# Performance work log

Hardware: AMD Instinct MI355X
Metric: run time of the kernel (lower is better)

## Reference

```python
import jax, jax.numpy as jnp
import numpy as np

V, E, H, S, B, T = 32000, 256, 512, 128, 32, 32


def setup_inputs() -> dict:
    key = jax.random.key(0)
    ks = iter(jax.random.split(key, 32))

    def w(shape, s=0.05):
        return jax.random.normal(next(ks), shape, dtype=jnp.float32) * s

    return dict(
        src=jax.random.randint(next(ks), (S, B), 0, V),
        trg=jax.random.randint(next(ks), (T, B), 0, V),
        embed=w((V, E)),
        enc_Wih_f=w((4 * H, E)), enc_Whh_f=w((4 * H, H)), enc_bih_f=w((4 * H,)), enc_bhh_f=w((4 * H,)),
        enc_Wih_b=w((4 * H, E)), enc_Whh_b=w((4 * H, H)), enc_bih_b=w((4 * H,)), enc_bhh_b=w((4 * H,)),
        attn_W=w((H, 2 * H)), attn_b=w((H,)), attn_v=w((H,)),
        dec_Wih0=w((4 * H, H + E)), dec_Whh0=w((4 * H, H)), dec_bih0=w((4 * H,)), dec_bhh0=w((4 * H,)),
        dec_Wih1=w((4 * H, H)), dec_Whh1=w((4 * H, H)), dec_bih1=w((4 * H,)), dec_bhh1=w((4 * H,)),
        out_W=w((V, 2 * H)), out_b=w((V,)),
    )


def _cell(x, h, c, Wih, Whh, bih, bhh):
    # PyTorch LSTM gate order: i, f, g, o
    z = x @ Wih.T + h @ Whh.T + bih + bhh
    i, f, g, o = jnp.split(z, 4, axis=-1)
    c2 = jax.nn.sigmoid(f) * c + jax.nn.sigmoid(i) * jnp.tanh(g)
    h2 = jax.nn.sigmoid(o) * jnp.tanh(c2)
    return h2, c2


def _run_lstm(xs, Wih, Whh, bih, bhh):
    # xs: [S, B, in]; returns outputs [S,B,H], final (h,c)
    h0 = jnp.zeros((xs.shape[1], Whh.shape[1]), xs.dtype)

    def step(carry, x):
        h, c = carry
        h2, c2 = _cell(x, h, c, Wih, Whh, bih, bhh)
        return (h2, c2), h2

    (hT, cT), outs = jax.lax.scan(step, (h0, h0), xs)
    return outs, hT, cT


def _forward(src, trg, embed,
             enc_Wih_f, enc_Whh_f, enc_bih_f, enc_bhh_f,
             enc_Wih_b, enc_Whh_b, enc_bih_b, enc_bhh_b,
             attn_W, attn_b, attn_v,
             dec_Wih0, dec_Whh0, dec_bih0, dec_bhh0,
             dec_Wih1, dec_Whh1, dec_bih1, dec_bhh1,
             out_W, out_b):
    emb_src = embed[src]                                  # [S,B,E]
    # bidirectional 1-layer encoder LSTM
    f_outs, hf, cf = _run_lstm(emb_src, enc_Wih_f, enc_Whh_f, enc_bih_f, enc_bhh_f)
    b_outs, hb, cb = _run_lstm(emb_src[::-1], enc_Wih_b, enc_Whh_b, enc_bih_b, enc_bhh_b)
    enc_out = f_outs + b_outs[::-1]                       # [S,B,H] (sum of directions)
    h = jnp.stack([hf, hb])                               # [2,B,H] -> decoder init state
    c = jnp.stack([cf, cb])
    enc_bsh = enc_out.transpose(1, 0, 2)                  # [B,S,H]

    def dec_step(carry, tok):
        h, c = carry
        emb = embed[tok]                                  # [B,E]
        q = h[-1]                                         # top-layer hidden [B,H]
        qs = jnp.broadcast_to(q[:, None, :], enc_bsh.shape)
        energy = jnp.tanh(jnp.concatenate([qs, enc_bsh], -1) @ attn_W.T + attn_b)  # [B,S,H]
        scores = energy @ attn_v                          # [B,S]
        aw = jax.nn.softmax(scores, axis=1)
        ctx = jnp.einsum('bs,bsh->bh', aw, enc_bsh)       # [B,H]
        x = jnp.concatenate([emb, ctx], -1)               # [B,E+H]
        h0, c0 = _cell(x, h[0], c[0], dec_Wih0, dec_Whh0, dec_bih0, dec_bhh0)
        h1, c1 = _cell(h0, h[1], c[1], dec_Wih1, dec_Whh1, dec_bih1, dec_bhh1)
        logits = jax.nn.log_softmax(
            jnp.concatenate([h1, ctx], -1) @ out_W.T + out_b, axis=-1)             # [B,V]
        return (jnp.stack([h0, h1]), jnp.stack([c0, c1])), logits

    # teacher forcing (ratio=1.0): input at step t is trg[t-1]
    _, outs = jax.lax.scan(dec_step, (h, c), trg[:-1])    # [T-1,B,V]
    outputs = jnp.concatenate(
        [jnp.zeros((1,) + outs.shape[1:], outs.dtype), outs], 0)  # outputs[0]=0 as in torch
    return outputs


def reference(src, trg, embed,
              enc_Wih_f, enc_Whh_f, enc_bih_f, enc_bhh_f,
              enc_Wih_b, enc_Whh_b, enc_bih_b, enc_bhh_b,
              attn_W, attn_b, attn_v,
              dec_Wih0, dec_Whh0, dec_bih0, dec_bhh0,
              dec_Wih1, dec_Whh1, dec_bih1, dec_bhh1,
              out_W, out_b):
    return _forward(src, trg, embed,
                    enc_Wih_f, enc_Whh_f, enc_bih_f, enc_bhh_f,
                    enc_Wih_b, enc_Whh_b, enc_bih_b, enc_bhh_b,
                    attn_W, attn_b, attn_v,
                    dec_Wih0, dec_Whh0, dec_bih0, dec_bhh0,
                    dec_Wih1, dec_Whh1, dec_bih1, dec_bhh1,
                    out_W, out_b)
```

## Files before the change

### kernel.cpp

```cpp
#include <hip/hip_runtime.h>
#include <stdint.h>


using short8 = __attribute__((ext_vector_type(8))) short;
using f32x4  = __attribute__((ext_vector_type(4))) float;
typedef _Float16 half2v __attribute__((ext_vector_type(2)));

__device__ __forceinline__ short f2bf(float x){
  unsigned u = __float_as_uint(x);
  unsigned r = (u + 0x7fffu + ((u >> 16) & 1u)) >> 16;
  return (short)(unsigned short)r;
}
__device__ __forceinline__ float bf2f_lo(unsigned u){ return __uint_as_float(u << 16); }
__device__ __forceinline__ float bf2f_hi(unsigned u){ return __uint_as_float(u & 0xffff0000u); }
__device__ __forceinline__ float sigmf(float x){ return 1.0f/(1.0f + __expf(-x)); }
__device__ __forceinline__ float fast_tanh(float x){
  const float e = __expf(2.0f*x);
  return 1.0f - 2.0f/(e + 1.0f);
}
__device__ __forceinline__ unsigned pack_h2(float a, float b){
  unsigned short ha = __builtin_bit_cast(unsigned short, (_Float16)a);
  unsigned short hb = __builtin_bit_cast(unsigned short, (_Float16)b);
  return (unsigned)ha | ((unsigned)hb << 16);
}
__device__ __forceinline__ float h2lo(unsigned u){ return (float)__builtin_bit_cast(half2v,u)[0]; }
__device__ __forceinline__ float h2hi(unsigned u){ return (float)__builtin_bit_cast(half2v,u)[1]; }
__device__ __forceinline__ float dot2u(unsigned x, unsigned w, float c){
#if __has_builtin(__builtin_amdgcn_fdot2)
  return __builtin_amdgcn_fdot2(__builtin_bit_cast(half2v,x), __builtin_bit_cast(half2v,w), c, false);
#else
  half2v hx = __builtin_bit_cast(half2v,x), hw = __builtin_bit_cast(half2v,w);
  c = fmaf((float)hx[0], (float)hw[0], c);
  c = fmaf((float)hx[1], (float)hw[1], c);
  return c;
#endif
}

__device__ __forceinline__ float4 load_coh_f4(const float* p){
  float4 v;
  asm volatile("global_load_dwordx4 %0, %1, off sc0 sc1\n\ts_waitcnt vmcnt(0)"
               : "=&v"(v) : "v"(p) : "memory");
  return v;
}
__device__ __forceinline__ uint4 load_coh_u4(const unsigned* p){
  uint4 v;
  asm volatile("global_load_dwordx4 %0, %1, off sc0 sc1\n\ts_waitcnt vmcnt(0)"
               : "=&v"(v) : "v"(p) : "memory");
  return v;
}
__device__ __forceinline__ void store_coh_u32(unsigned* p, unsigned v){
  asm volatile("global_store_dword %0, %1, off sc0 sc1" :: "v"(p), "v"(v) : "memory");
}
__device__ __forceinline__ void store_coh_f32(float* p, float v){
  asm volatile("global_store_dword %0, %1, off sc0 sc1" :: "v"(p), "v"(v) : "memory");
}

__device__ __forceinline__ void wait_spread(const unsigned* base, int n, unsigned target){
  if (threadIdx.x < 64){
    const bool mine = (int)threadIdx.x < n;
    const unsigned* p = base + (threadIdx.x << 4);
    for(;;){
      unsigned v = target;
      if (mine)
        asm volatile("global_load_dword %0, %1, off sc0 sc1\n\ts_waitcnt vmcnt(0)"
                     : "=&v"(v) : "v"(p) : "memory");
      if (__all(v >= target)) break;
    }
  }
  __syncthreads();
}
__device__ __forceinline__ void set_flag_sp(unsigned* slot, unsigned val){
  asm volatile("s_waitcnt vmcnt(0)" ::: "memory");
  __syncthreads();
  if (threadIdx.x == 0) store_coh_u32(slot, val);
}

__device__ __forceinline__ void stage8u(const unsigned* src, int bg8, unsigned* lds){
  const unsigned* s0 = src + (size_t)bg8*2048;
  const int f0 = threadIdx.x, f1 = f0 + 256;
  uint4 a, b;
  asm volatile(
    "global_load_dwordx4 %0, %2, off sc0 sc1\n\t"
    "global_load_dwordx4 %1, %3, off sc0 sc1\n\t"
    "s_waitcnt vmcnt(0)"
    : "=&v"(a), "=&v"(b)
    : "v"(s0 + (f0<<2)), "v"(s0 + (f1<<2))
    : "memory");
  { const int row = f0>>6, cu = (f0&63)<<2; *(uint4*)&lds[row*260+cu] = a; }
  { const int row = f1>>6, cu = (f1&63)<<2; *(uint4*)&lds[row*260+cu] = b; }
}

__device__ __forceinline__ void stage4u(const unsigned* src, int bg4, unsigned* lds){
  const unsigned* s0 = src + (size_t)bg4*1024;
  uint4 a;
  asm volatile(
    "global_load_dwordx4 %0, %1, off sc0 sc1\n\ts_waitcnt vmcnt(0)"
    : "=&v"(a) : "v"(s0 + (threadIdx.x<<2)) : "memory");
  const int row = threadIdx.x>>6, cu = (threadIdx.x&63)<<2;
  *(uint4*)&lds[row*260+cu] = a;
}

__device__ __forceinline__ float dot512(const unsigned* xrow, const unsigned* w){
  float a = 0.f;
  #pragma unroll 4
  for (int it = 0; it < 16; ++it){
    uint4 x0 = *(const uint4*)(xrow + it*16);
    uint4 x1 = *(const uint4*)(xrow + it*16 + 4);
    uint4 x2 = *(const uint4*)(xrow + it*16 + 8);
    uint4 x3 = *(const uint4*)(xrow + it*16 + 12);
    uint4 w0 = *(const uint4*)(w + it*16);
    uint4 w1 = *(const uint4*)(w + it*16 + 4);
    uint4 w2 = *(const uint4*)(w + it*16 + 8);
    uint4 w3 = *(const uint4*)(w + it*16 + 12);
    a = dot2u(x0.x,w0.x,a); a = dot2u(x0.y,w0.y,a); a = dot2u(x0.z,w0.z,a); a = dot2u(x0.w,w0.w,a);
    a = dot2u(x1.x,w1.x,a); a = dot2u(x1.y,w1.y,a); a = dot2u(x1.z,w1.z,a); a = dot2u(x1.w,w1.w,a);
    a = dot2u(x2.x,w2.x,a); a = dot2u(x2.y,w2.y,a); a = dot2u(x2.z,w2.z,a); a = dot2u(x2.w,w2.w,a);
    a = dot2u(x3.x,w3.x,a); a = dot2u(x3.y,w3.y,a); a = dot2u(x3.z,w3.z,a); a = dot2u(x3.w,w3.w,a);
  }
  return a;
}

__device__ __forceinline__ float2 dot2rows(const unsigned* xrow, const unsigned* wA, const unsigned* wB){
  float a = 0.f, b = 0.f;
  #pragma unroll 8
  for (int it = 0; it < 32; ++it){
    uint4 x0 = *(const uint4*)(xrow + it*8);
    uint4 x1 = *(const uint4*)(xrow + it*8 + 4);
    uint4 a0 = *(const uint4*)(wA + it*8);
    uint4 a1 = *(const uint4*)(wA + it*8 + 4);
    uint4 b0 = *(const uint4*)(wB + it*8);
    uint4 b1 = *(const uint4*)(wB + it*8 + 4);
    a = dot2u(x0.x,a0.x,a); a = dot2u(x0.y,a0.y,a); a = dot2u(x0.z,a0.z,a); a = dot2u(x0.w,a0.w,a);
    a = dot2u(x1.x,a1.x,a); a = dot2u(x1.y,a1.y,a); a = dot2u(x1.z,a1.z,a); a = dot2u(x1.w,a1.w,a);
    b = dot2u(x0.x,b0.x,b); b = dot2u(x0.y,b0.y,b); b = dot2u(x0.z,b0.z,b); b = dot2u(x0.w,b0.w,b);
    b = dot2u(x1.x,b1.x,b); b = dot2u(x1.y,b1.y,b); b = dot2u(x1.z,b1.z,b); b = dot2u(x1.w,b1.w,b);
  }
  return make_float2(a, b);
}

__global__ void k_zero(float* __restrict__ p, int n){
  int i = blockIdx.x*256 + threadIdx.x;
  const int stride = gridDim.x*256;
  for (; i < n; i += stride) p[i] = 0.f;
}

__global__ __launch_bounds__(256) void k_cvt_f16(const float* __restrict__ s, unsigned short* __restrict__ d, int n){
  int i = blockIdx.x*256 + threadIdx.x;
  const int stride = gridDim.x*256;
  for (; i < n; i += stride) d[i] = __builtin_bit_cast(unsigned short, (_Float16)s[i]);
}
__global__ __launch_bounds__(256) void k_cvt_f16_str(const float* __restrict__ s, int lds_, unsigned short* __restrict__ d, int n){
  int i = blockIdx.x*256 + threadIdx.x;
  const int stride = gridDim.x*256;
  for (; i < n; i += stride){
    const int row = i >> 9, c = i & 511;
    d[i] = __builtin_bit_cast(unsigned short, (_Float16)s[(size_t)row*lds_ + c]);
  }
}

__global__ __launch_bounds__(256) void k_gather(
    const int* __restrict__ src, const int* __restrict__ trg,
    const float* __restrict__ embed,
    short* __restrict__ emb_src_bf, short* __restrict__ emb_trg_bf)
{
  const int row = blockIdx.x, tid = threadIdx.x;
  if (row < 4096){
    const int tok = src[row];
    emb_src_bf[(size_t)row*256 + tid] = f2bf(embed[(size_t)tok*256 + tid]);
  } else {
    const int r = row - 4096;
    short v = 0;
    if (r < 992){ const int tok = trg[r]; v = f2bf(embed[(size_t)tok*256 + tid]); }
    emb_trg_bf[(size_t)r*256 + tid] = v;
  }
}

__global__ __launch_bounds__(256) void k_gemm_aw(
    const short* __restrict__ A, int lda,
    const float* __restrict__ W, int ldw,
    float* __restrict__ C, int ldc,
    const float* __restrict__ bias0, const float* __restrict__ bias1,
    int Mvalid, int K, int tmode, short* __restrict__ Cbf)
{
  __shared__ __align__(16) short As[128*32];
  __shared__ __align__(16) short Bs[128*32];
  const int tid = threadIdx.x;
  const int bm = blockIdx.x, bn = blockIdx.y;
  const int w  = tid >> 6,  l  = tid & 63;
  const int wm = w >> 1,    wn = w & 1;
  const int lr = l & 15,    lk = l >> 4;

  const int r0 = tid >> 2;
  const int s0 = (tid & 3) << 3;
  const int r1 = r0 + 64;

  const short* a0 = A + (size_t)(bm*128 + r0)*lda + s0;
  const short* a1 = A + (size_t)(bm*128 + r1)*lda + s0;
  const float* w0 = W + (size_t)(bn*128 + r0)*ldw + s0;
  const float* w1 = W + (size_t)(bn*128 + r1)*ldw + s0;

  const f32x4 zero4 = {0.f,0.f,0.f,0.f};
  f32x4 acc[4][4];
  #pragma unroll
  for (int mi=0;mi<4;mi++){
    #pragma unroll
    for (int ni=0;ni<4;ni++) acc[mi][ni] = zero4;
  }

  for (int k0 = 0; k0 < K; k0 += 32){
    short8 va0 = *(const short8*)(a0 + k0);
    short8 va1 = *(const short8*)(a1 + k0);
    float4 f00 = *(const float4*)(w0 + k0);
    float4 f01 = *(const float4*)(w0 + k0 + 4);
    float4 f10 = *(const float4*)(w1 + k0);
    float4 f11 = *(const float4*)(w1 + k0 + 4);
    short8 vb0, vb1;
    vb0[0]=f2bf(f00.x); vb0[1]=f2bf(f00.y); vb0[2]=f2bf(f00.z); vb0[3]=f2bf(f00.w);
    vb0[4]=f2bf(f01.x); vb0[5]=f2bf(f01.y); vb0[6]=f2bf(f01.z); vb0[7]=f2bf(f01.w);
    vb1[0]=f2bf(f10.x); vb1[1]=f2bf(f10.y); vb1[2]=f2bf(f10.z); vb1[3]=f2bf(f10.w);
    vb1[4]=f2bf(f11.x); vb1[5]=f2bf(f11.y); vb1[6]=f2bf(f11.z); vb1[7]=f2bf(f11.w);

    __syncthreads();
    *((short8*)As + tid)       = va0;
    *((short8*)As + tid + 256) = va1;
    *((short8*)Bs + tid)       = vb0;
    *((short8*)Bs + tid + 256) = vb1;
    __syncthreads();

    short8 af[4], bfr[4];
    #pragma unroll
    for (int mi=0;mi<4;mi++) af[mi]  = *(const short8*)&As[(wm*64 + mi*16 + lr)*32 + (lk<<3)];
    #pragma unroll
    for (int ni=0;ni<4;ni++) bfr[ni] = *(const short8*)&Bs[(wn*64 + ni*16 + lr)*32 + (lk<<3)];
    #pragma unroll
    for (int mi=0;mi<4;mi++){
      #pragma unroll
      for (int ni=0;ni<4;ni++)
        acc[mi][ni] = __builtin_amdgcn_mfma_f32_16x16x32_bf16(af[mi], bfr[ni], acc[mi][ni], 0,0,0);
    }
  }

  #pragma unroll
  for (int mi=0;mi<4;mi++){
    const int rb = bm*128 + wm*64 + mi*16 + (lk<<2);
    #pragma unroll
    for (int ni=0;ni<4;ni++){
      const int col = bn*128 + wn*64 + ni*16 + lr;
      float bv = 0.f;
      if (bias0) bv += bias0[col];
      if (bias1) bv += bias1[col];
      #pragma unroll
      for (int rr=0;rr<4;rr++){
        const int row = rb + rr;
        if (row < Mvalid){
          const float vv = acc[mi][ni][rr] + bv;
          if (Cbf)        Cbf[(size_t)row*ldc + col] = f2bf(vv);
          else if (tmode) C[(size_t)(row>>5)*65536 + (size_t)col*32 + (row&31)] = vv;
          else            C[(size_t)row*ldc + col] = vv;
        }
      }
    }
  }
}

__global__ __launch_bounds__(256,1) void k_enc_persist(
    const float* __restrict__ pre_f, const float* __restrict__ pre_b,
    const unsigned short* __restrict__ WhF, const unsigned short* __restrict__ WhB,
    unsigned* __restrict__ f_outs, unsigned* __restrict__ b_outs,
    float* __restrict__ c_f_out, float* __restrict__ c_b_out,
    unsigned* __restrict__ eflag)
{
  __shared__ __align__(16) unsigned x_lds[8*260];
  __shared__ float zbuf[64*8];
  const int bid = blockIdx.x, tid = threadIdx.x;
  const int x = bid & 7, m = bid >> 3;
  const int dir = m & 1, bg = (m >> 1) & 3, q = m >> 3;
  const int jb = x*4 + q;
  const float* pre = dir ? pre_b : pre_f;
  const unsigned* Wh = (const unsigned*)(dir ? WhB : WhF);
  unsigned* outs = dir ? b_outs : f_outs;
  float* c_out = dir ? c_b_out : c_f_out;
  unsigned* flags = eflag + (size_t)(dir*4 + bg)*512;

  const int bb = tid & 7, rr = tid >> 3;
  const int g = rr >> 3, op = rr & 7;
  const unsigned* wA = Wh + (size_t)(g*512 + jb*16 + 2*op)*256;
  const unsigned* wB = wA + 256;

  const int fo = tid & 15, fb = tid >> 4;
  const int b_out = bg*8 + fb, k_out = jb*16 + fo;
  float c_reg = 0.f;

  for (int t = 0; t < 128; ++t){
    float pz[4];
    if (tid < 128){
      const int tt = dir ? (127 - t) : t;
      const float* pt = pre + (size_t)tt*65536;
      #pragma unroll
      for (int gg = 0; gg < 4; ++gg)
        pz[gg] = pt[(size_t)(gg*512 + k_out)*32 + b_out];
    }
    if (t){
      wait_spread(flags, 32, (unsigned)t);
      stage8u(outs + (size_t)(t-1)*8192, bg, x_lds);
    } else {
      for (int i = tid; i < 8*260; i += 256) x_lds[i] = 0;
    }
    __syncthreads();

    const float2 d = dot2rows(x_lds + bb*260, wA, wB);
    zbuf[(g*16 + 2*op)*8 + bb]   = d.x;
    zbuf[(g*16 + 2*op+1)*8 + bb] = d.y;
    __syncthreads();

    if (tid < 128){
      float z[4];
      #pragma unroll
      for (int gg = 0; gg < 4; ++gg)
        z[gg] = pz[gg] + zbuf[(gg*16 + fo)*8 + fb];
      const float cn = sigmf(z[1])*c_reg + sigmf(z[0])*fast_tanh(z[2]);
      c_reg = cn;
      const float hn = sigmf(z[3])*fast_tanh(cn);
      const unsigned pu = pack_h2(hn, __shfl_xor(hn, 1));
      if (!(tid & 1))
        store_coh_u32(outs + (size_t)t*8192 + (size_t)b_out*256 + (k_out>>1), pu);
    }
    set_flag_sp(flags + jb*16, (unsigned)(t+1));
  }
  if (tid < 128) c_out[b_out*512 + k_out] = c_reg;
}

__global__ __launch_bounds__(256) void k_sum_enc(
    const unsigned* __restrict__ f_o, const unsigned* __restrict__ b_o,
    unsigned* __restrict__ enc_sum_bf_u)
{
  const int i = blockIdx.x*256 + threadIdx.x;
  const int s = i >> 13, rem = i & 8191;
  const unsigned a = f_o[i], b = b_o[(size_t)(127 - s)*8192 + rem];
  const float lo = h2lo(a) + h2lo(b);
  const float hi = h2hi(a) + h2hi(b);
  enc_sum_bf_u[i] = (unsigned)(unsigned short)f2bf(lo) | ((unsigned)(unsigned short)f2bf(hi) << 16);
}

__global__ __launch_bounds__(256,1) void k_dec_persist(
    const float* __restrict__ demb,
    const unsigned short* __restrict__ Wih0h,
    const unsigned short* __restrict__ Whh0h,
    const unsigned short* __restrict__ Wih1h,
    const unsigned short* __restrict__ Whh1h,
    const float* __restrict__ bih1, const float* __restrict__ bhh1,
    const unsigned short* __restrict__ wqh,
    const float* __restrict__ attnV,
    const short* __restrict__ enc_proj_bf,
    const unsigned* __restrict__ enc_sum_u,
    const unsigned* __restrict__ h0i, const unsigned* __restrict__ h1i,
    const float* __restrict__ c0_init, const float* __restrict__ c1_init,
    unsigned* __restrict__ h0buf, unsigned* __restrict__ h1buf,
    unsigned* __restrict__ ctxb,
    float* __restrict__ qsb,
    short* __restrict__ h1ctx,
    unsigned* __restrict__ flagQ, unsigned* __restrict__ flagH0,
    unsigned* __restrict__ flagH1, unsigned* __restrict__ flagCtx)
{
  __shared__ __align__(16) unsigned x1s[4*260];
  __shared__ __align__(16) unsigned x0s[4*260];
  __shared__ float zfin[64*5];
  __shared__ __align__(16) float q_s[512], v_s[512];
  __shared__ float part[256], aw[128], red[128];

  const int bid = blockIdx.x, tid = threadIdx.x;
  const int x = bid & 7, m = bid >> 3;
  const int bg = m & 7, q = m >> 3;
  const int jb = x*4 + q;
  const bool is_attn = ((jb & 7) == 0);
  const int ar = jb >> 3;
  const int ab = bg*4 + ar;

  unsigned* fQ  = flagQ  + bg*512;
  unsigned* fH0 = flagH0 + bg*512;
  unsigned* fH1 = flagH1 + bg*512;
  unsigned* fCt = flagCtx + bg*64;

  const int b  = tid & 3;
  const int jr = tid >> 2;
  const int g  = jr >> 4, col = jr & 15;
  const int j_row = g*512 + jb*16 + col;

  const int fcol = tid & 15, fb2 = tid >> 4;
  const int b_out = bg*4 + fb2, k_out = jb*16 + fcol;

  const unsigned* Wh0row = (const unsigned*)Whh0h + (size_t)j_row*256;
  const unsigned* Wh1row = (const unsigned*)Whh1h + (size_t)j_row*256;
  const unsigned* Wi0row = (const unsigned*)Wih0h + (size_t)j_row*256;
  const unsigned* Wi1row = (const unsigned*)Wih1h + (size_t)j_row*256;
  const unsigned* WQu    = (const unsigned*)wqh;

  float c0_reg = 0.f, c1_reg = 0.f, bias1g[4];
  if (tid < 64){
    c0_reg = c0_init[b_out*512 + k_out];
    c1_reg = c1_init[b_out*512 + k_out];
    #pragma unroll
    for (int gg=0; gg<4; ++gg) bias1g[gg] = bih1[gg*512 + k_out] + bhh1[gg*512 + k_out];
  }
  if (is_attn && tid < 128) ((float4*)v_s)[tid] = ((const float4*)attnV)[tid];

  float zh0 = 0.f;

  for (int t = 0; t < 31; ++t){
    const float demb_v = demb[(size_t)t*65536 + (size_t)j_row*32 + bg*4 + b];

    if (t){
      wait_spread(fH1, 32, (unsigned)t);
      stage4u(h1buf + (size_t)(t&1)*8192, bg, x1s);
    } else {
      stage4u(h1i, bg, x1s);
      stage4u(h0i, bg, x0s);
    }
    __syncthreads();
    if (t == 0) zh0 = dot512(x0s + b*260, Wh0row);
    const float zh1 = dot512(x1s + b*260, Wh1row);
    if (tid < 64){
      const int qb = tid >> 4, qcol = jb*16 + (tid & 15);
      const float qv = dot512(x1s + qb*260, WQu + (size_t)qcol*256);
      store_coh_f32(qsb + (size_t)(bg*4 + qb)*512 + qcol, qv);
    }
    set_flag_sp(fQ + jb*16, (unsigned)(t+1));

    if (is_attn){
      wait_spread(fQ, 32, (unsigned)(t+1));
      if (tid < 128) ((float4*)q_s)[tid] = load_coh_f4(qsb + (size_t)ab*512 + (tid<<2));
      __syncthreads();
      {
        const int s = tid >> 1, half = tid & 1;
        const unsigned* ep = (const unsigned*)(enc_proj_bf + ((size_t)(s*32 + ab))*512 + (half << 8));
        const float* qh = q_s + (half << 8);
        const float* vh = v_s + (half << 8);
        float p = 0.f;
        for (int kk = 0; kk < 128; kk += 4){
          uint4 e = *(const uint4*)(ep + kk);
          const int k2 = kk << 1;
          p += fast_tanh(qh[k2+0] + bf2f_lo(e.x)) * vh[k2+0];
          p += fast_tanh(qh[k2+1] + bf2f_hi(e.x)) * vh[k2+1];
          p += fast_tanh(qh[k2+2] + bf2f_lo(e.y)) * vh[k2+2];
          p += fast_tanh(qh[k2+3] + bf2f_hi(e.y)) * vh[k2+3];
          p += fast_tanh(qh[k2+4] + bf2f_lo(e.z)) * vh[k2+4];
          p += fast_tanh(qh[k2+5] + bf2f_hi(e.z)) * vh[k2+5];
          p += fast_tanh(qh[k2+6] + bf2f_lo(e.w)) * vh[k2+6];
          p += fast_tanh(qh[k2+7] + bf2f_hi(e.w)) * vh[k2+7];
        }
        part[tid] = p;
      }
      __syncthreads();
      if (tid < 128){ const float sc = part[2*tid] + part[2*tid+1]; aw[tid] = sc; red[tid] = sc; }
      __syncthreads();
      for (int off = 64; off > 0; off >>= 1){
        if (tid < off) red[tid] = fmaxf(red[tid], red[tid+off]);
        __syncthreads();
      }
      const float mx = red[0];
      __syncthreads();
      if (tid < 128){ const float e = __expf(aw[tid] - mx); aw[tid] = e; red[tid] = e; }
      __syncthreads();
      for (int off = 64; off > 0; off >>= 1){
        if (tid < off) red[tid] += red[tid+off];
        __syncthreads();
      }
      const float inv = 1.0f / red[0];
      if (tid < 128) aw[tid] *= inv;
      __syncthreads();
      {
        const int cc = tid << 1;
        float x0 = 0.f, x1 = 0.f;
        for (int s2 = 0; s2 < 128; ++s2){
          const unsigned u = enc_sum_u[(size_t)(s2*32 + ab)*256 + tid];
          const float a = aw[s2];
          x0 = fmaf(a, bf2f_lo(u), x0);
          x1 = fmaf(a, bf2f_hi(u), x1);
        }
        store_coh_u32(ctxb + (size_t)ab*256 + tid, pack_h2(x0, x1));
        h1ctx[(size_t)t*32768 + ab*1024 + 512 + cc]     = f2bf(x0);
        h1ctx[(size_t)t*32768 + ab*1024 + 512 + cc + 1] = f2bf(x1);
      }
      set_flag_sp(fCt + ar*16, (unsigned)(t+1));
    }

    wait_spread(fCt, 4, (unsigned)(t+1));
    stage4u(ctxb, bg, x0s);
    __syncthreads();
    zfin[jr*5 + b] = demb_v + dot512(x0s + b*260, Wi0row) + zh0;
    __syncthreads();
    if (tid < 64){
      float z[4];
      #pragma unroll
      for (int gg=0; gg<4; ++gg) z[gg] = zfin[(gg*16 + fcol)*5 + fb2];
      const float cn = sigmf(z[1])*c0_reg + sigmf(z[0])*fast_tanh(z[2]);
      c0_reg = cn;
      const float hn = sigmf(z[3])*fast_tanh(cn);
      const unsigned pu = pack_h2(hn, __shfl_xor(hn, 1));
      if (!(tid & 1))
        store_coh_u32(h0buf + (size_t)((t+1)&1)*8192 + (size_t)b_out*256 + (k_out>>1), pu);
    }
    set_flag_sp(fH0 + jb*16, (unsigned)(t+1));

    wait_spread(fH0, 32, (unsigned)(t+1));
    stage4u(h0buf + (size_t)((t+1)&1)*8192, bg, x1s);
    __syncthreads();
    {
      const float2 d = dot2rows(x1s + b*260, Wi1row, Wh0row);
      zfin[jr*5 + b] = d.x + zh1;
      zh0 = d.y;
    }
    __syncthreads();
    if (tid < 64){
      float z[4];
      #pragma unroll
      for (int gg=0; gg<4; ++gg) z[gg] = bias1g[gg] + zfin[(gg*16 + fcol)*5 + fb2];
      const float cn = sigmf(z[1])*c1_reg + sigmf(z[0])*fast_tanh(z[2]);
      c1_reg = cn;
      const float hn = sigmf(z[3])*fast_tanh(cn);
      const unsigned pu = pack_h2(hn, __shfl_xor(hn, 1));
      if (!(tid & 1))
        store_coh_u32(h1buf + (size_t)((t+1)&1)*8192 + (size_t)b_out*256 + (k_out>>1), pu);
      h1ctx[(size_t)t*32768 + (size_t)b_out*1024 + k_out] = f2bf(hn);
    }
    set_flag_sp(fH1 + jb*16, (unsigned)(t+1));
  }
}

__global__ __launch_bounds__(256) void k_logsm(float* __restrict__ out){
  float* row = out + (size_t)blockIdx.x * 32000;
  const int tid = threadIdx.x;
  __shared__ float red[256];
  float s = 0.f;
  for (int i = tid; i < 8000; i += 256){
    const float4 v = ((const float4*)row)[i];
    s += __expf(v.x) + __expf(v.y) + __expf(v.z) + __expf(v.w);
  }
  red[tid] = s; __syncthreads();
  for (int off = 128; off > 0; off >>= 1){
    if (tid < off) red[tid] += red[tid+off];
    __syncthreads();
  }
  const float lse = __logf(red[0]);
  for (int i = tid; i < 8000; i += 256){
    float4 v = ((const float4*)row)[i];
    v.x -= lse; v.y -= lse; v.z -= lse; v.w -= lse;
    ((float4*)row)[i] = v;
  }
}

extern "C" void kernel_launch(void* const* d_in, const int* in_sizes, int n_in,
                              void* d_out, int out_size, void* d_ws, size_t ws_size,
                              hipStream_t stream)
{
  (void)in_sizes; (void)n_in; (void)out_size; (void)ws_size;
  const int*   src   = (const int*)d_in[0];
  const int*   trg   = (const int*)d_in[1];
  const float* embed = (const float*)d_in[2];
  const float* eWihF = (const float*)d_in[3];
  const float* eWhhF = (const float*)d_in[4];
  const float* ebihF = (const float*)d_in[5];
  const float* ebhhF = (const float*)d_in[6];
  const float* eWihB = (const float*)d_in[7];
  const float* eWhhB = (const float*)d_in[8];
  const float* ebihB = (const float*)d_in[9];
  const float* ebhhB = (const float*)d_in[10];
  const float* attnW = (const float*)d_in[11];
  const float* attnB = (const float*)d_in[12];
  const float* attnV = (const float*)d_in[13];
  const float* dWih0 = (const float*)d_in[14];
  const float* dWhh0 = (const float*)d_in[15];
  const float* dbih0 = (const float*)d_in[16];
  const float* dbhh0 = (const float*)d_in[17];
  const float* dWih1 = (const float*)d_in[18];
  const float* dWhh1 = (const float*)d_in[19];
  const float* dbih1 = (const float*)d_in[20];
  const float* dbhh1 = (const float*)d_in[21];
  const float* outW  = (const float*)d_in[22];
  const float* outB  = (const float*)d_in[23];

  float* out = (float*)d_out;
  float* enc_in_f = out;
  float* enc_in_b = out + 8388608;
  short* enc_proj_bf = (short*)(out + 18874368);
  unsigned* f_outs = (unsigned*)(out + 20971520);
  unsigned* b_outs = (unsigned*)(out + 23068672);
  float* demb     = out + 25165824;
  short* emb_src_bf = (short*)(out + 27262976);
  short* emb_trg_bf = (short*)(out + 27787264);
  unsigned* enc_sum_bf_u = (unsigned*)(out + 27918336);
  unsigned short* wqh    = (unsigned short*)(out + 28966912);
  unsigned short* whhF_h = (unsigned short*)(out + 29229056);
  unsigned short* whhB_h = (unsigned short*)(out + 29753344);
  unsigned short* wih0_h = (unsigned short*)(out + 30277632);
  unsigned short* whh0_h = (unsigned short*)(out + 30801920);
  unsigned short* wih1_h = (unsigned short*)(out + 31326208);
  unsigned short* whh1_h = (unsigned short*)(out + 31850496);
  float* qsb            = out + 32374784;

  char* ws = (char*)d_ws;
  short* h1ctx = (short*)ws;
  unsigned* h0buf = (unsigned*)(ws + 2097152);
  unsigned* h1buf = (unsigned*)(ws + 2162688);
  unsigned* ctxb  = (unsigned*)(ws + 2228224);
  float* c_f      = (float*)(ws + 2260992);
  float* c_b      = (float*)(ws + 2326528);
  unsigned* eflag   = (unsigned*)(ws + 2392064);
  unsigned* flagQ   = (unsigned*)(ws + 2408448);
  unsigned* flagH0  = (unsigned*)(ws + 2424832);
  unsigned* flagH1  = (unsigned*)(ws + 2441216);
  unsigned* flagCtx = (unsigned*)(ws + 2457600);

  k_zero<<<8, 256, 0, stream>>>((float*)eflag, 16896);
  k_gather<<<5120, 256, 0, stream>>>(src, trg, embed, emb_src_bf, emb_trg_bf);
  {
    dim3 g1(32,16);
    k_gemm_aw<<<g1,256,0,stream>>>(emb_src_bf,256, eWihF,256, enc_in_f,2048, ebihF,ebhhF, 4096,256, 1, nullptr);
    k_gemm_aw<<<g1,256,0,stream>>>(emb_src_bf,256, eWihB,256, enc_in_b,2048, ebihB,ebhhB, 4096,256, 1, nullptr);
    dim3 g2(8,16);
    k_gemm_aw<<<g2,256,0,stream>>>(emb_trg_bf,256, dWih0,768, demb,2048, dbih0,dbhh0, 1024,256, 1, nullptr);
  }
  k_cvt_f16<<<1024,256,0,stream>>>(eWhhF, whhF_h, 1048576);
  k_cvt_f16<<<1024,256,0,stream>>>(eWhhB, whhB_h, 1048576);
  k_cvt_f16_str<<<1024,256,0,stream>>>(dWih0+256, 768, wih0_h, 1048576);
  k_cvt_f16<<<1024,256,0,stream>>>(dWhh0, whh0_h, 1048576);
  k_cvt_f16<<<1024,256,0,stream>>>(dWih1, wih1_h, 1048576);
  k_cvt_f16<<<1024,256,0,stream>>>(dWhh1, whh1_h, 1048576);
  k_cvt_f16_str<<<256,256,0,stream>>>(attnW, 1024, wqh, 262144);
  k_enc_persist<<<256, 256, 0, stream>>>(enc_in_f, enc_in_b, whhF_h, whhB_h,
                                         f_outs, b_outs, c_f, c_b, eflag);
  k_sum_enc<<<4096, 256, 0, stream>>>(f_outs, b_outs, enc_sum_bf_u);
  {
    dim3 g3(32,4);
    k_gemm_aw<<<g3,256,0,stream>>>((const short*)enc_sum_bf_u,512, attnW+512,1024, nullptr,512, attnB,nullptr, 4096,512, 0, enc_proj_bf);
  }
  k_dec_persist<<<256, 256, 0, stream>>>(demb, wih0_h, whh0_h, wih1_h, whh1_h,
                                         dbih1, dbhh1, wqh, attnV, enc_proj_bf,
                                         enc_sum_bf_u,
                                         f_outs + (size_t)127*8192, b_outs + (size_t)127*8192,
                                         c_f, c_b, h0buf, h1buf, ctxb, qsb, h1ctx,
                                         flagQ, flagH0, flagH1, flagCtx);
  k_zero<<<512, 256, 0, stream>>>(out, 1024000);
  {
    dim3 g4(8,250);
    k_gemm_aw<<<g4,256,0,stream>>>(h1ctx,1024, outW,1024, out + 1024000, 32000, outB,nullptr, 992,1024, 0, nullptr);
  }
  k_logsm<<<992, 256, 0, stream>>>(out + 1024000);
}
```

Measured before the change: 2.410 ms.

## Split decoder attention into dedicated blocks and drop a barrier from flag publishing

The persistent decoder is launched with 32 extra blocks, each computing the attention query, scores, softmax and context for one batch row. This replaces the old scheme where selected LSTM blocks computed the query cooperatively and exchanged it through a global buffer with an extra flag phase. The LSTM blocks now overlap their layer-1 recurrent dot with the attention work and wait only on the context flag. Cell updates use half as many threads, each handling two hidden units, and flag publishing drops its __syncthreads. Polling moves to the last wavefront. The risks are ordering bugs from the removed barrier and each attention block recomputing the full 512-wide query.

New measurement: 2.991 ms. 1.24x slower.

```diff
diff --git a/kernel.cpp b/kernel.cpp
--- a/kernel.cpp
+++ b/kernel.cpp
@@ -10,6 +10,9 @@
   unsigned u = __float_as_uint(x);
   unsigned r = (u + 0x7fffu + ((u >> 16) & 1u)) >> 16;
   return (short)(unsigned short)r;
+}
+__device__ __forceinline__ unsigned bfpair(float a, float b){
+  return (unsigned)(unsigned short)f2bf(a) | ((unsigned)(unsigned short)f2bf(b) << 16);
 }
 __device__ __forceinline__ float bf2f_lo(unsigned u){ return __uint_as_float(u << 16); }
 __device__ __forceinline__ float bf2f_hi(unsigned u){ return __uint_as_float(u & 0xffff0000u); }
@@ -36,12 +39,6 @@
 #endif
 }
 
-__device__ __forceinline__ float4 load_coh_f4(const float* p){
-  float4 v;
-  asm volatile("global_load_dwordx4 %0, %1, off sc0 sc1\n\ts_waitcnt vmcnt(0)"
-               : "=&v"(v) : "v"(p) : "memory");
-  return v;
-}
 __device__ __forceinline__ uint4 load_coh_u4(const unsigned* p){
   uint4 v;
   asm volatile("global_load_dwordx4 %0, %1, off sc0 sc1\n\ts_waitcnt vmcnt(0)"
@@ -51,14 +48,12 @@
 __device__ __forceinline__ void store_coh_u32(unsigned* p, unsigned v){
   asm volatile("global_store_dword %0, %1, off sc0 sc1" :: "v"(p), "v"(v) : "memory");
 }
-__device__ __forceinline__ void store_coh_f32(float* p, float v){
-  asm volatile("global_store_dword %0, %1, off sc0 sc1" :: "v"(p), "v"(v) : "memory");
-}
-
-__device__ __forceinline__ void wait_spread(const unsigned* base, int n, unsigned target){
-  if (threadIdx.x < 64){
-    const bool mine = (int)threadIdx.x < n;
-    const unsigned* p = base + (threadIdx.x << 4);
+
+__device__ __forceinline__ void wait_w3(const unsigned* base, int n, unsigned target){
+  if (threadIdx.x >= 192){
+    const int l = threadIdx.x - 192;
+    const bool mine = l < n;
+    const unsigned* p = base + (l << 4);
     for(;;){
       unsigned v = target;
       if (mine)
@@ -69,9 +64,8 @@
   }
   __syncthreads();
 }
-__device__ __forceinline__ void set_flag_sp(unsigned* slot, unsigned val){
+__device__ __forceinline__ void publish(unsigned* slot, unsigned val){
   asm volatile("s_waitcnt vmcnt(0)" ::: "memory");
-  __syncthreads();
   if (threadIdx.x == 0) store_coh_u32(slot, val);
 }
 
@@ -287,21 +281,24 @@
   const unsigned* wA = Wh + (size_t)(g*512 + jb*16 + 2*op)*256;
   const unsigned* wB = wA + 256;
 
-  const int fo = tid & 15, fb = tid >> 4;
-  const int b_out = bg*8 + fb, k_out = jb*16 + fo;
-  float c_reg = 0.f;
+  const int cp = tid & 7, fb = tid >> 3;
+  const int b_out = bg*8 + fb;
+  const int k0 = jb*16 + 2*cp;
+  float c_a = 0.f, c_b2 = 0.f;
 
   for (int t = 0; t < 128; ++t){
-    float pz[4];
-    if (tid < 128){
+    float pz[8];
+    if (tid < 64){
       const int tt = dir ? (127 - t) : t;
       const float* pt = pre + (size_t)tt*65536;
       #pragma unroll
-      for (int gg = 0; gg < 4; ++gg)
-        pz[gg] = pt[(size_t)(gg*512 + k_out)*32 + b_out];
+      for (int gg = 0; gg < 4; ++gg){
+        pz[gg]   = pt[(size_t)(gg*512 + k0)*32 + b_out];
+        pz[gg+4] = pt[(size_t)(gg*512 + k0 + 1)*32 + b_out];
+      }
     }
     if (t){
-      wait_spread(flags, 32, (unsigned)t);
+      wait_w3(flags, 32, (unsigned)t);
       stage8u(outs + (size_t)(t-1)*8192, bg, x_lds);
     } else {
       for (int i = tid; i < 8*260; i += 256) x_lds[i] = 0;
@@ -313,21 +310,26 @@
     zbuf[(g*16 + 2*op+1)*8 + bb] = d.y;
     __syncthreads();
 
-    if (tid < 128){
-      float z[4];
+    if (tid < 64){
+      float za[4], zb[4];
       #pragma unroll
-      for (int gg = 0; gg < 4; ++gg)
-        z[gg] = pz[gg] + zbuf[(gg*16 + fo)*8 + fb];
-      const float cn = sigmf(z[1])*c_reg + sigmf(z[0])*fast_tanh(z[2]);
-      c_reg = cn;
-      const float hn = sigmf(z[3])*fast_tanh(cn);
-      const unsigned pu = pack_h2(hn, __shfl_xor(hn, 1));
-      if (!(tid & 1))
-        store_coh_u32(outs + (size_t)t*8192 + (size_t)b_out*256 + (k_out>>1), pu);
-    }
-    set_flag_sp(flags + jb*16, (unsigned)(t+1));
-  }
-  if (tid < 128) c_out[b_out*512 + k_out] = c_reg;
+      for (int gg = 0; gg < 4; ++gg){
+        za[gg] = pz[gg]   + zbuf[(gg*16 + 2*cp)*8 + fb];
+        zb[gg] = pz[gg+4] + zbuf[(gg*16 + 2*cp+1)*8 + fb];
+      }
+      const float ca = sigmf(za[1])*c_a  + sigmf(za[0])*fast_tanh(za[2]);
+      const float cb = sigmf(zb[1])*c_b2 + sigmf(zb[0])*fast_tanh(zb[2]);
+      c_a = ca; c_b2 = cb;
+      const float ha = sigmf(za[3])*fast_tanh(ca);
+      const float hb = sigmf(zb[3])*fast_tanh(cb);
+      store_coh_u32(outs + (size_t)t*8192 + (size_t)b_out*256 + (k0>>1), pack_h2(ha, hb));
+    }
+    publish(flags + jb*16, (unsigned)(t+1));
+  }
+  if (tid < 64){
+    c_out[b_out*512 + k0]     = c_a;
+    c_out[b_out*512 + k0 + 1] = c_b2;
+  }
 }
 
 __global__ __launch_bounds__(256) void k_sum_enc(
@@ -339,7 +341,7 @@
   const unsigned a = f_o[i], b = b_o[(size_t)(127 - s)*8192 + rem];
   const float lo = h2lo(a) + h2lo(b);
   const float hi = h2hi(a) + h2hi(b);
-  enc_sum_bf_u[i] = (unsigned)(unsigned short)f2bf(lo) | ((unsigned)(unsigned short)f2bf(hi) << 16);
+  enc_sum_bf_u[i] = bfpair(lo, hi);
 }
 
 __global__ __launch_bounds__(256,1) void k_dec_persist(
@@ -357,82 +359,40 @@
     const float* __restrict__ c0_init, const float* __restrict__ c1_init,
     unsigned* __restrict__ h0buf, unsigned* __restrict__ h1buf,
     unsigned* __restrict__ ctxb,
-    float* __restrict__ qsb,
     short* __restrict__ h1ctx,
-    unsigned* __restrict__ flagQ, unsigned* __restrict__ flagH0,
-    unsigned* __restrict__ flagH1, unsigned* __restrict__ flagCtx)
+    unsigned* __restrict__ fH1, unsigned* __restrict__ fH0, unsigned* __restrict__ fCtx)
 {
   __shared__ __align__(16) unsigned x1s[4*260];
   __shared__ __align__(16) unsigned x0s[4*260];
   __shared__ float zfin[64*5];
+  __shared__ __align__(16) unsigned h1l[256];
   __shared__ __align__(16) float q_s[512], v_s[512];
   __shared__ float part[256], aw[128], red[128];
 
   const int bid = blockIdx.x, tid = threadIdx.x;
-  const int x = bid & 7, m = bid >> 3;
-  const int bg = m & 7, q = m >> 3;
-  const int jb = x*4 + q;
-  const bool is_attn = ((jb & 7) == 0);
-  const int ar = jb >> 3;
-  const int ab = bg*4 + ar;
-
-  unsigned* fQ  = flagQ  + bg*512;
-  unsigned* fH0 = flagH0 + bg*512;
-  unsigned* fH1 = flagH1 + bg*512;
-  unsigned* fCt = flagCtx + bg*64;
-
-  const int b  = tid & 3;
-  const int jr = tid >> 2;
-  const int g  = jr >> 4, col = jr & 15;
-  const int j_row = g*512 + jb*16 + col;
-
-  const int fcol = tid & 15, fb2 = tid >> 4;
-  const int b_out = bg*4 + fb2, k_out = jb*16 + fcol;
-
-  const unsigned* Wh0row = (const unsigned*)Whh0h + (size_t)j_row*256;
-  const unsigned* Wh1row = (const unsigned*)Whh1h + (size_t)j_row*256;
-  const unsigned* Wi0row = (const unsigned*)Wih0h + (size_t)j_row*256;
-  const unsigned* Wi1row = (const unsigned*)Wih1h + (size_t)j_row*256;
-  const unsigned* WQu    = (const unsigned*)wqh;
-
-  float c0_reg = 0.f, c1_reg = 0.f, bias1g[4];
-  if (tid < 64){
-    c0_reg = c0_init[b_out*512 + k_out];
-    c1_reg = c1_init[b_out*512 + k_out];
-    #pragma unroll
-    for (int gg=0; gg<4; ++gg) bias1g[gg] = bih1[gg*512 + k_out] + bhh1[gg*512 + k_out];
-  }
-  if (is_attn && tid < 128) ((float4*)v_s)[tid] = ((const float4*)attnV)[tid];
-
-  float zh0 = 0.f;
-
-  for (int t = 0; t < 31; ++t){
-    const float demb_v = demb[(size_t)t*65536 + (size_t)j_row*32 + bg*4 + b];
-
-    if (t){
-      wait_spread(fH1, 32, (unsigned)t);
-      stage4u(h1buf + (size_t)(t&1)*8192, bg, x1s);
-    } else {
-      stage4u(h1i, bg, x1s);
-      stage4u(h0i, bg, x0s);
-    }
-    __syncthreads();
-    if (t == 0) zh0 = dot512(x0s + b*260, Wh0row);
-    const float zh1 = dot512(x1s + b*260, Wh1row);
-    if (tid < 64){
-      const int qb = tid >> 4, qcol = jb*16 + (tid & 15);
-      const float qv = dot512(x1s + qb*260, WQu + (size_t)qcol*256);
-      store_coh_f32(qsb + (size_t)(bg*4 + qb)*512 + qcol, qv);
-    }
-    set_flag_sp(fQ + jb*16, (unsigned)(t+1));
-
-    if (is_attn){
-      wait_spread(fQ, 32, (unsigned)(t+1));
-      if (tid < 128) ((float4*)q_s)[tid] = load_coh_f4(qsb + (size_t)ab*512 + (tid<<2));
+
+  if (bid >= 256){
+    const int b = bid - 256;
+    const int bg = b >> 2;
+    unsigned* myH1 = fH1 + bg*512;
+    if (tid < 128) ((float4*)v_s)[tid] = ((const float4*)attnV)[tid];
+    __syncthreads();
+
+    for (int t = 0; t < 31; ++t){
+      if (t) wait_w3(myH1, 32, (unsigned)t);
+      else   __syncthreads();
+      const unsigned* hsrc = (t==0 ? h1i : h1buf + (size_t)(t&1)*8192) + (size_t)b*256;
+      if (tid < 64) *(uint4*)&h1l[tid<<2] = load_coh_u4(hsrc + (tid<<2));
+      __syncthreads();
+      {
+        const float2 qq = dot2rows(h1l, (const unsigned*)wqh + (size_t)tid*256,
+                                        (const unsigned*)wqh + (size_t)(tid+256)*256);
+        q_s[tid] = qq.x; q_s[tid+256] = qq.y;
+      }
       __syncthreads();
       {
         const int s = tid >> 1, half = tid & 1;
-        const unsigned* ep = (const unsigned*)(enc_proj_bf + ((size_t)(s*32 + ab))*512 + (half << 8));
+        const unsigned* ep = (const unsigned*)(enc_proj_bf + ((size_t)(s*32 + b))*512 + (half << 8));
         const float* qh = q_s + (half << 8);
         const float* vh = v_s + (half << 8);
         float p = 0.f;
@@ -468,62 +428,127 @@
       const float inv = 1.0f / red[0];
       if (tid < 128) aw[tid] *= inv;
       __syncthreads();
-      {
-        const int cc = tid << 1;
-        float x0 = 0.f, x1 = 0.f;
+      if (tid < 64){
+        const unsigned* es = enc_sum_u + (size_t)b*256 + (tid<<2);
+        float c0=0,c1=0,c2=0,c3=0,c4=0,c5=0,c6=0,c7=0;
         for (int s2 = 0; s2 < 128; ++s2){
-          const unsigned u = enc_sum_u[(size_t)(s2*32 + ab)*256 + tid];
           const float a = aw[s2];
-          x0 = fmaf(a, bf2f_lo(u), x0);
-          x1 = fmaf(a, bf2f_hi(u), x1);
+          uint4 u = *(const uint4*)(es + (size_t)s2*8192);
+          c0 = fmaf(a, bf2f_lo(u.x), c0); c1 = fmaf(a, bf2f_hi(u.x), c1);
+          c2 = fmaf(a, bf2f_lo(u.y), c2); c3 = fmaf(a, bf2f_hi(u.y), c3);
+          c4 = fmaf(a, bf2f_lo(u.z), c4); c5 = fmaf(a, bf2f_hi(u.z), c5);
+          c6 = fmaf(a, bf2f_lo(u.w), c6); c7 = fmaf(a, bf2f_hi(u.w), c7);
         }
-        store_coh_u32(ctxb + (size_t)ab*256 + tid, pack_h2(x0, x1));
-        h1ctx[(size_t)t*32768 + ab*1024 + 512 + cc]     = f2bf(x0);
-        h1ctx[(size_t)t*32768 + ab*1024 + 512 + cc + 1] = f2bf(x1);
-      }
-      set_flag_sp(fCt + ar*16, (unsigned)(t+1));
-    }
-
-    wait_spread(fCt, 4, (unsigned)(t+1));
+        unsigned* cp4 = ctxb + (size_t)b*256 + (tid<<2);
+        store_coh_u32(cp4+0, pack_h2(c0,c1));
+        store_coh_u32(cp4+1, pack_h2(c2,c3));
+        store_coh_u32(cp4+2, pack_h2(c4,c5));
+        store_coh_u32(cp4+3, pack_h2(c6,c7));
+        unsigned* hc = (unsigned*)h1ctx + ((size_t)t*16384 + (size_t)b*512 + 256 + (tid<<2));
+        hc[0] = bfpair(c0,c1); hc[1] = bfpair(c2,c3); hc[2] = bfpair(c4,c5); hc[3] = bfpair(c6,c7);
+      }
+      publish(fCtx + b*16, (unsigned)(t+1));
+    }
+    return;
+  }
+
+  const int x = bid & 7, m = bid >> 3;
+  const int bg = m & 7, q = m >> 3;
+  const int jb = x*4 + q;
+
+  unsigned* grpH1 = fH1 + bg*512;
+  unsigned* grpH0 = fH0 + bg*512;
+  unsigned* grpCt = fCtx + bg*64;
+
+  const int b = tid & 3;
+  const int jr = tid >> 2;
+  const int g  = jr >> 4, col = jr & 15;
+  const int j_row = g*512 + jb*16 + col;
+
+  const int cp = tid & 7, fb2 = tid >> 3;
+  const int b_out = bg*4 + fb2;
+  const int k0 = jb*16 + 2*cp;
+
+  const unsigned* Wh0row = (const unsigned*)Whh0h + (size_t)j_row*256;
+  const unsigned* Wh1row = (const unsigned*)Whh1h + (size_t)j_row*256;
+  const unsigned* Wi0row = (const unsigned*)Wih0h + (size_t)j_row*256;
+  const unsigned* Wi1row = (const unsigned*)Wih1h + (size_t)j_row*256;
+
+  float c0a = 0.f, c0b = 0.f, c1a = 0.f, c1b = 0.f;
+  float b1a[4], b1b[4];
+  if (tid < 32){
+    c0a = c0_init[b_out*512 + k0];   c0b = c0_init[b_out*512 + k0 + 1];
+    c1a = c1_init[b_out*512 + k0];   c1b = c1_init[b_out*512 + k0 + 1];
+    #pragma unroll
+    for (int gg=0; gg<4; ++gg){
+      b1a[gg] = bih1[gg*512 + k0]     + bhh1[gg*512 + k0];
+      b1b[gg] = bih1[gg*512 + k0 + 1] + bhh1[gg*512 + k0 + 1];
+    }
+  }
+  __syncthreads();
+
+  float zh0 = 0.f;
+
+  for (int t = 0; t < 31; ++t){
+    const float demb_v = demb[(size_t)t*65536 + (size_t)j_row*32 + bg*4 + b];
+
+    if (t){
+      wait_w3(grpH1, 32, (unsigned)t);
+      stage4u(h1buf + (size_t)(t&1)*8192, bg, x1s);
+    } else {
+      stage4u(h1i, bg, x1s);
+      stage4u(h0i, bg, x0s);
+    }
+    __syncthreads();
+    if (t == 0) zh0 = dot512(x0s + b*260, Wh0row);
+    const float zh1 = dot512(x1s + b*260, Wh1row);
+
+    wait_w3(grpCt, 4, (unsigned)(t+1));
     stage4u(ctxb, bg, x0s);
     __syncthreads();
     zfin[jr*5 + b] = demb_v + dot512(x0s + b*260, Wi0row) + zh0;
     __syncthreads();
-    if (tid < 64){
-      float z[4];
+    if (tid < 32){
+      float za[4], zb[4];
       #pragma unroll
-      for (int gg=0; gg<4; ++gg) z[gg] = zfin[(gg*16 + fcol)*5 + fb2];
-      const float cn = sigmf(z[1])*c0_reg + sigmf(z[0])*fast_tanh(z[2]);
-      c0_reg = cn;
-      const float hn = sigmf(z[3])*fast_tanh(cn);
-      const unsigned pu = pack_h2(hn, __shfl_xor(hn, 1));
-      if (!(tid & 1))
-        store_coh_u32(h0buf + (size_t)((t+1)&1)*8192 + (size_t)b_out*256 + (k_out>>1), pu);
-    }
-    set_flag_sp(fH0 + jb*16, (unsigned)(t+1));
-
-    wait_spread(fH0, 32, (unsigned)(t+1));
-    stage4u(h0buf + (size_t)((t+1)&1)*8192, bg, x1s);
+      for (int gg=0; gg<4; ++gg){
+        za[gg] = zfin[(gg*16 + 2*cp)*5 + fb2];
+        zb[gg] = zfin[(gg*16 + 2*cp+1)*5 + fb2];
+      }
+      const float ca = sigmf(za[1])*c0a + sigmf(za[0])*fast_tanh(za[2]);
+      const float cb = sigmf(zb[1])*c0b + sigmf(zb[0])*fast_tanh(zb[2]);
+      c0a = ca; c0b = cb;
+      const float ha = sigmf(za[3])*fast_tanh(ca);
+      const float hb = sigmf(zb[3])*fast_tanh(cb);
+      store_coh_u32(h0buf + (size_t)((t+1)&1)*8192 + (size_t)b_out*256 + (k0>>1), pack_h2(ha, hb));
+    }
+    publish(grpH0 + jb*16, (unsigned)(t+1));
+
+    wait_w3(grpH0, 32, (unsigned)(t+1));
+    stage4u(h0buf + (size_t)((t+1)&1)*8192, bg, x0s);
     __syncthreads();
     {
-      const float2 d = dot2rows(x1s + b*260, Wi1row, Wh0row);
+      const float2 d = dot2rows(x0s + b*260, Wi1row, Wh0row);
       zfin[jr*5 + b] = d.x + zh1;
       zh0 = d.y;
     }
     __syncthreads();
-    if (tid < 64){
-      float z[4];
+    if (tid < 32){
+      float za[4], zb[4];
       #pragma unroll
-      for (int gg=0; gg<4; ++gg) z[gg] = bias1g[gg] + zfin[(gg*16 + fcol)*5 + fb2];
-      const float cn = sigmf(z[1])*c1_reg + sigmf(z[0])*fast_tanh(z[2]);
-      c1_reg = cn;
-      const float hn = sigmf(z[3])*fast_tanh(cn);
-      const unsigned pu = pack_h2(hn, __shfl_xor(hn, 1));
-      if (!(tid & 1))
-        store_coh_u32(h1buf + (size_t)((t+1)&1)*8192 + (size_t)b_out*256 + (k_out>>1), pu);
-      h1ctx[(size_t)t*32768 + (size_t)b_out*1024 + k_out] = f2bf(hn);
-    }
-    set_flag_sp(fH1 + jb*16, (unsigned)(t+1));
+      for (int gg=0; gg<4; ++gg){
+        za[gg] = b1a[gg] + zfin[(gg*16 + 2*cp)*5 + fb2];
+        zb[gg] = b1b[gg] + zfin[(gg*16 + 2*cp+1)*5 + fb2];
+      }
+      const float ca = sigmf(za[1])*c1a + sigmf(za[0])*fast_tanh(za[2]);
+      const float cb = sigmf(zb[1])*c1b + sigmf(zb[0])*fast_tanh(zb[2]);
+      c1a = ca; c1b = cb;
+      const float ha = sigmf(za[3])*fast_tanh(ca);
+      const float hb = sigmf(zb[3])*fast_tanh(cb);
+      store_coh_u32(h1buf + (size_t)((t+1)&1)*8192 + (size_t)b_out*256 + (k0>>1), pack_h2(ha, hb));
+      ((unsigned*)h1ctx)[(size_t)t*16384 + (size_t)b_out*512 + (k0>>1)] = bfpair(ha, hb);
+    }
+    publish(grpH1 + jb*16, (unsigned)(t+1));
   }
 }
 
@@ -596,7 +621,6 @@
   unsigned short* whh0_h = (unsigned short*)(out + 30801920);
   unsigned short* wih1_h = (unsigned short*)(out + 31326208);
   unsigned short* whh1_h = (unsigned short*)(out + 31850496);
-  float* qsb            = out + 32374784;
 
   char* ws = (char*)d_ws;
   short* h1ctx = (short*)ws;
@@ -605,13 +629,12 @@
   unsigned* ctxb  = (unsigned*)(ws + 2228224);
   float* c_f      = (float*)(ws + 2260992);
   float* c_b      = (float*)(ws + 2326528);
-  unsigned* eflag   = (unsigned*)(ws + 2392064);
-  unsigned* flagQ   = (unsigned*)(ws + 2408448);
-  unsigned* flagH0  = (unsigned*)(ws + 2424832);
-  unsigned* flagH1  = (unsigned*)(ws + 2441216);
-  unsigned* flagCtx = (unsigned*)(ws + 2457600);
-
-  k_zero<<<8, 256, 0, stream>>>((float*)eflag, 16896);
+  unsigned* eflag = (unsigned*)(ws + 2392064);
+  unsigned* fH1   = (unsigned*)(ws + 2408448);
+  unsigned* fH0   = (unsigned*)(ws + 2424832);
+  unsigned* fCtx  = (unsigned*)(ws + 2441216);
+
+  k_zero<<<8, 256, 0, stream>>>((float*)eflag, 12800);
   k_gather<<<5120, 256, 0, stream>>>(src, trg, embed, emb_src_bf, emb_trg_bf);
   {
     dim3 g1(32,16);
@@ -634,12 +657,12 @@
     dim3 g3(32,4);
     k_gemm_aw<<<g3,256,0,stream>>>((const short*)enc_sum_bf_u,512, attnW+512,1024, nullptr,512, attnB,nullptr, 4096,512, 0, enc_proj_bf);
   }
-  k_dec_persist<<<256, 256, 0, stream>>>(demb, wih0_h, whh0_h, wih1_h, whh1_h,
+  k_dec_persist<<<288, 256, 0, stream>>>(demb, wih0_h, whh0_h, wih1_h, whh1_h,
                                          dbih1, dbhh1, wqh, attnV, enc_proj_bf,
                                          enc_sum_bf_u,
                                          f_outs + (size_t)127*8192, b_outs + (size_t)127*8192,
-                                         c_f, c_b, h0buf, h1buf, ctxb, qsb, h1ctx,
-                                         flagQ, flagH0, flagH1, flagCtx);
+                                         c_f, c_b, h0buf, h1buf, ctxb, h1ctx,
+                                         fH1, fH0, fCtx);
   k_zero<<<512, 256, 0, stream>>>(out, 1024000);
   {
     dim3 g4(8,250);
```
